# Kernel optimization log

Hardware: AMD Instinct MI355X
Metric: run time of the kernel (lower is better)

The kernel has to match this reference:

```python
import jax, jax.numpy as jnp
import numpy as np

EMBED_DIM = 768
NUM_HEADS = 12
LN_EPS = 1e-5


def _apply_rope3d(p16, e):
    """3-axis RoPE. p16: [B,1,L,3] float16 coords; e: [B,H,L,D] float32.
    Heads split into 3 groups (x/y/z); within each group last dim split in halves
    and rotated by angle coord*freqs (computed in fp16, matching the .half() cast)."""
    B, H, L, D = e.shape
    half = D // 2
    freqs = (10000.0 ** (-jnp.arange(half, dtype=jnp.float32) / half)).astype(jnp.float16)
    ang = p16[..., None] * freqs                     # [B,1,L,3,half] fp16
    ang = jnp.transpose(ang, (0, 3, 1, 2, 4))        # [B,3,1,L,half]
    c, s = jnp.cos(ang), jnp.sin(ang)                # fp16
    eg = e.reshape(B, 3, H // 3, L, D)               # 3 head groups
    e1, e2 = eg[..., :half], eg[..., half:]
    o1 = e1 * c - e2 * s                             # fp16*fp32 -> fp32
    o2 = e2 * c + e1 * s
    return jnp.concatenate([o1, o2], axis=-1).reshape(B, H, L, D)


def setup_inputs() -> dict:
    key = jax.random.key(0)
    ks = jax.random.split(key, 5)
    B, L, C = 4, 2048, EMBED_DIM
    feat = jax.random.normal(ks[0], (B, L, C), dtype=jnp.float32)
    pos = jax.random.normal(ks[1], (B, L, 3), dtype=jnp.float32)
    w_qkv = jax.random.normal(ks[2], (C, 3 * C), dtype=jnp.float32) * (1.0 / np.sqrt(C))
    b_qkv = jnp.zeros((3 * C,), dtype=jnp.float32)
    w_proj = jax.random.normal(ks[3], (C, C), dtype=jnp.float32) * (1.0 / np.sqrt(C))
    b_proj = jnp.zeros((C,), dtype=jnp.float32)
    ln_g = jnp.ones((C,), dtype=jnp.float32)
    ln_b = jnp.zeros((C,), dtype=jnp.float32)
    return {"feat": feat, "pos": pos, "ln_g": ln_g, "ln_b": ln_b,
            "w_qkv": w_qkv, "b_qkv": b_qkv, "w_proj": w_proj, "b_proj": b_proj}


def reference(feat, pos, ln_g, ln_b, w_qkv, b_qkv, w_proj, b_proj):
    B, L, C = feat.shape
    H = NUM_HEADS
    D = C // H
    # LayerNorm
    mu = jnp.mean(feat, axis=-1, keepdims=True)
    var = jnp.mean(jnp.square(feat - mu), axis=-1, keepdims=True)
    x = (feat - mu) * jax.lax.rsqrt(var + LN_EPS) * ln_g + ln_b
    # QKV projection and head split
    qkv = x @ w_qkv + b_qkv
    q, k, v = jnp.split(qkv, 3, axis=-1)
    q = q.reshape(B, L, H, D).transpose(0, 2, 1, 3)  # [B,H,L,D]
    k = k.reshape(B, L, H, D).transpose(0, 2, 1, 3)
    v = v.reshape(B, L, H, D).transpose(0, 2, 1, 3)
    # 3D-coordinate RoPE (angles in fp16 per original .half() cast)
    p16 = pos.astype(jnp.float16)[:, None]           # [B,1,L,3]
    q = _apply_rope3d(p16, q)
    k = _apply_rope3d(p16, k)
    # flex_attention with block_mask=None -> full softmax attention, scale 1/sqrt(D)
    scale = 1.0 / np.sqrt(D)
    att = jax.nn.softmax(jnp.einsum('bhqd,bhkd->bhqk', q, k) * scale, axis=-1)
    out = jnp.einsum('bhqk,bhkd->bhqd', att, v)
    out = out.transpose(0, 2, 1, 3).reshape(B, L, C)
    # output projection (dropout = identity in eval)
    return out @ w_proj + b_proj
```

## Files before the change

kernel.cpp:

```cpp
#include <hip/hip_runtime.h>

typedef unsigned short u16;
typedef unsigned int u32;
typedef __attribute__((ext_vector_type(8))) __bf16 bf16x8;
typedef __attribute__((ext_vector_type(4))) __bf16 bf16x4;
typedef __attribute__((ext_vector_type(8))) u16 ushort8;
typedef __attribute__((ext_vector_type(4))) float f32x4;

#define DEV static __device__ __forceinline__

DEV float bf2f(u16 v) { union { u32 u; float f; } x; x.u = ((u32)v) << 16; return x.f; }
DEV u16 f2bf(float f) {
  u32 u = __builtin_bit_cast(u32, f);
  return (u16)((u + 0x7fffu + ((u >> 16) & 1u)) >> 16);
}
DEV float rnd_bf(float f) { return bf2f(f2bf(f)); }
DEV u32 pack2(float a, float b) { return (u32)f2bf(a) | ((u32)f2bf(b) << 16); }

DEV void gload_lds16(const void* g, void* l) {
  __builtin_amdgcn_global_load_lds((const __attribute__((address_space(1))) u32*)g,
                                   (__attribute__((address_space(3))) u32*)l, 16, 0, 0);
}

DEV f32x4 MFMA16(bf16x8 a, bf16x8 b, f32x4 c) {
  return __builtin_amdgcn_mfma_f32_16x16x32_bf16(a, b, c, 0, 0, 0);
}

#define QSCALE (0.125f * 1.442695040888963f)

__global__ __launch_bounds__(256) void prep_kernel(const float* __restrict__ pos, float2* __restrict__ tab,
                                                   const float* __restrict__ w_qkv, u16* __restrict__ wqkvT,
                                                   const float* __restrict__ w_proj, u16* __restrict__ wprojT,
                                                   const float* __restrict__ feat, const float* __restrict__ gam,
                                                   const float* __restrict__ bet, u16* __restrict__ xo) {
  __shared__ u16 t[64][65];
  const int tid = threadIdx.x;
  const int blk = blockIdx.x;

  if (blk < 3072) {
    int gid = blk * 256 + tid;
    int row = gid & 8191;
    int ad = gid >> 13;
    int axis = ad >> 5, d = ad & 31;
    float p = pos[(size_t)row * 3 + axis];
    float fr = exp2f((float)d * -0.41524101186092029f);
    _Float16 ah = (_Float16)p * (_Float16)fr;
    float sn, cs;
    sincosf((float)ah, &sn, &cs);
    tab[gid] = make_float2((float)(_Float16)cs, (float)(_Float16)sn);
  } else if (blk < 3648) {
    const float* W;
    u16* Wt;
    int rows = 768, cols, bx, by;
    if (blk < 3504) {
      int i2 = blk - 3072;
      W = w_qkv; Wt = wqkvT; cols = 2304; bx = i2 % 36; by = i2 / 36;
    } else {
      int i2 = blk - 3504;
      W = w_proj; Wt = wprojT; cols = 768; bx = i2 % 12; by = i2 / 12;
    }
    const int tr = by << 6, tc = bx << 6;
    {
      int r = tid >> 2, c0 = (tid & 3) << 4;
      const float* src = W + (size_t)(tr + r) * cols + tc + c0;
#pragma unroll
      for (int i = 0; i < 16; i += 4) {
        float4 v = *(const float4*)(src + i);
        t[r][c0 + i]     = f2bf(v.x);
        t[r][c0 + i + 1] = f2bf(v.y);
        t[r][c0 + i + 2] = f2bf(v.z);
        t[r][c0 + i + 3] = f2bf(v.w);
      }
    }
    __syncthreads();
    {
      int dd = tid >> 2, l0 = (tid & 3) << 4;
      ushort8 o0, o1;
#pragma unroll
      for (int i = 0; i < 8; ++i) { o0[i] = t[l0 + i][dd]; o1[i] = t[l0 + 8 + i][dd]; }
      u16* dst = Wt + (size_t)(tc + dd) * rows + tr + l0;
      *(ushort8*)dst = o0;
      *(ushort8*)(dst + 8) = o1;
    }
  } else {
    const int row = (blk - 3648) * 4 + (tid >> 6);
    const int lane = tid & 63;
    const float* f = feat + (size_t)row * 768 + lane * 4;
    float4 v0 = *(const float4*)f;
    float4 v1 = *(const float4*)(f + 256);
    float4 v2 = *(const float4*)(f + 512);
    float s = v0.x + v0.y + v0.z + v0.w + v1.x + v1.y + v1.z + v1.w + v2.x + v2.y + v2.z + v2.w;
    float s2 = v0.x*v0.x + v0.y*v0.y + v0.z*v0.z + v0.w*v0.w
             + v1.x*v1.x + v1.y*v1.y + v1.z*v1.z + v1.w*v1.w
             + v2.x*v2.x + v2.y*v2.y + v2.z*v2.z + v2.w*v2.w;
#pragma unroll
    for (int off = 32; off > 0; off >>= 1) { s += __shfl_xor(s, off); s2 += __shfl_xor(s2, off); }
    const float mu = s * (1.0f / 768.0f);
    const float rstd = rsqrtf(s2 * (1.0f / 768.0f) - mu * mu + 1e-5f);
    u16* o = xo + (size_t)row * 768 + lane * 4;
    const float4* gp = (const float4*)(gam + lane * 4);
    const float4* bp = (const float4*)(bet + lane * 4);
    float4 vv[3] = {v0, v1, v2};
#pragma unroll
    for (int jj = 0; jj < 3; ++jj) {
      float4 gg = gp[jj * 64];
      float4 bb = bp[jj * 64];
      uint2 pk;
      pk.x = pack2((vv[jj].x - mu) * rstd * gg.x + bb.x, (vv[jj].y - mu) * rstd * gg.y + bb.y);
      pk.y = pack2((vv[jj].z - mu) * rstd * gg.z + bb.z, (vv[jj].w - mu) * rstd * gg.w + bb.w);
      *(uint2*)(o + jj * 256) = pk;
    }
  }
}

template<bool ROPE, bool F32OUT, int TM>
__global__ __launch_bounds__(256) void gemm_bt(const u16* __restrict__ A, const u16* __restrict__ Bt,
                                               const float* __restrict__ bias, void* __restrict__ Cout,
                                               u16* __restrict__ Qb, u16* __restrict__ Kb,
                                               const float2* __restrict__ tab, int M, int N, int K) {
  __shared__ u16 lds[TM * 64 + 8192];
  constexpr int MF = TM / 32;
  const int tid = threadIdx.x;
  const int lane = tid & 63, wv = tid >> 6;
  const int l16 = lane & 15, g = lane >> 4;
  const int nt = N >> 7;
  int bid = (int)blockIdx.x;
  { const int cpx = (int)gridDim.x >> 3; bid = (bid & 7) * cpx + (bid >> 3); }
  const int bm = bid / nt, bn = bid % nt;
  const int m0 = bm * TM, n0 = bn << 7;
  const int wr = (wv >> 1) * (TM / 2), wc = (wv & 1) << 6;
  const int rl = wv * 8 + (lane >> 3);
  const int slot = lane & 7;

  f32x4 acc[MF][4] = {};

  for (int k0 = 0; k0 < K; k0 += 64) {
    __syncthreads();
#pragma unroll
    for (int it = 0; it < TM / 32; ++it) {
      int r = it * 32 + rl;
      gload_lds16(A + (size_t)(m0 + r) * K + k0 + 8 * (slot ^ (r & 7)),
                  (char*)lds + it * 4096 + wv * 1024);
    }
#pragma unroll
    for (int it = 0; it < 4; ++it) {
      int r = it * 32 + rl;
      gload_lds16(Bt + (size_t)(n0 + r) * K + k0 + 8 * (slot ^ (r & 7)),
                  (char*)lds + TM * 128 + it * 4096 + wv * 1024);
    }
    __syncthreads();
#pragma unroll
    for (int ks = 0; ks < 2; ++ks) {
      bf16x8 af[MF], bfr[4];
#pragma unroll
      for (int mf = 0; mf < MF; ++mf) {
        int r = wr + mf * 16 + l16;
        af[mf] = *(const bf16x8*)((const char*)lds + r * 128 + ((ks * 64 + g * 16) ^ ((r & 7) << 4)));
      }
#pragma unroll
      for (int nf = 0; nf < 4; ++nf) {
        int r = wc + nf * 16 + l16;
        bfr[nf] = *(const bf16x8*)((const char*)lds + TM * 128 + r * 128 + ((ks * 64 + g * 16) ^ ((r & 7) << 4)));
      }
#pragma unroll
      for (int mf = 0; mf < MF; ++mf)
#pragma unroll
        for (int nf = 0; nf < 4; ++nf)
          acc[mf][nf] = MFMA16(af[mf], bfr[nf], acc[mf][nf]);
    }
  }

  bool ropePath = false;
  if constexpr (ROPE) ropePath = (n0 < 1536);
  if (ropePath) {
    if constexpr (ROPE) {
      const int colbase = n0 + wc;
      const bool isQ = colbase < 768;
      const int h = (isQ ? colbase : colbase - 768) >> 6;
      const int axis = h >> 2;
      u16* P = isQ ? Qb : Kb;
#pragma unroll
      for (int nf = 0; nf < 2; ++nf) {
        const int col = n0 + wc + nf * 16 + l16;
        const int d = nf * 16 + l16;
        const float2* trow = tab + (size_t)(axis * 32 + d) * 8192;
        const float b1 = bias[col], b2 = bias[col + 32];
#pragma unroll
        for (int mf = 0; mf < MF; ++mf) {
          int row0 = m0 + wr + mf * 16 + g * 4;
#pragma unroll
          for (int j = 0; j < 4; ++j) {
            int row = row0 + j;
            float2 cs2 = trow[row];
            float c = cs2.x, s = cs2.y;
            float a = acc[mf][nf][j] + b1;
            float bb = acc[mf][nf + 2][j] + b2;
            float o1 = a * c - bb * s;
            float o2 = bb * c + a * s;
            if (isQ) { o1 *= QSCALE; o2 *= QSCALE; }
            size_t obase = ((size_t)((row >> 11) * 12 + h) * 2048 + (row & 2047)) * 64;
            P[obase + d]      = f2bf(o1);
            P[obase + d + 32] = f2bf(o2);
          }
        }
      }
    }
  } else {
    const int colsub = (ROPE ? 1536 : 0);
    const int Nout = (ROPE ? 768 : N);
#pragma unroll
    for (int nf = 0; nf < 4; ++nf) {
      int col = n0 + wc + nf * 16 + l16;
      float bb = bias[col];
#pragma unroll
      for (int mf = 0; mf < MF; ++mf) {
        int row = m0 + wr + mf * 16 + g * 4;
#pragma unroll
        for (int j = 0; j < 4; ++j) {
          float v = acc[mf][nf][j] + bb;
          if (F32OUT) ((float*)Cout)[(size_t)(row + j) * Nout + col - colsub] = rnd_bf(v);
          else        ((u16*)Cout)[(size_t)(row + j) * Nout + col - colsub] = f2bf(v);
        }
      }
    }
  }
}

__global__ __launch_bounds__(256) void v_transpose(const u16* __restrict__ Vp, u16* __restrict__ Vt) {
  __shared__ u16 t[64][65];
  const int tid = threadIdx.x;
  const int lt = blockIdx.x, bh = blockIdx.y;
  const int b = bh / 12, h = bh - b * 12;
  {
    int r = tid >> 2, c0 = (tid & 3) << 4;
    const u16* src = Vp + (size_t)(b * 2048 + lt * 64 + r) * 768 + h * 64 + c0;
    ushort8 a0 = *(const ushort8*)src;
    ushort8 a1 = *(const ushort8*)(src + 8);
#pragma unroll
    for (int i = 0; i < 8; ++i) { t[r][c0 + i] = a0[i]; t[r][c0 + 8 + i] = a1[i]; }
  }
  __syncthreads();
  {
    int dd = tid >> 2, l0 = (tid & 3) << 4;
    ushort8 o0, o1;
#pragma unroll
    for (int i = 0; i < 8; ++i) { o0[i] = t[l0 + i][dd]; o1[i] = t[l0 + 8 + i][dd]; }
    u16* dst = Vt + (size_t)(bh * 64 + dd) * 2048 + lt * 64 + l0;
    *(ushort8*)dst = o0;
    *(ushort8*)(dst + 8) = o1;
  }
}

__global__ __launch_bounds__(256) void attn_kernel(const u16* __restrict__ Q, const u16* __restrict__ K,
                                                   const u16* __restrict__ Vt, u16* __restrict__ O) {
  __shared__ u16 kv_lds[3][8192];
  const int tid = threadIdx.x;
  const int lane = tid & 63, wv = tid >> 6;
  const int l16 = lane & 15, g = lane >> 4;
  int bid = (int)blockIdx.x;
  bid = (bid & 7) * 96 + (bid >> 3);
  const int bh = bid >> 4;
  const int q0 = (bid & 15) * 128 + wv * 32;
  const size_t base = (size_t)bh * (2048 * 64);
  const size_t vbase = (size_t)bh * (64 * 2048);
  const int rl = wv * 8 + (lane >> 3);
  const int slot = lane & 7;

  bf16x8 qf[2][2];
#pragma unroll
  for (int qm = 0; qm < 2; ++qm)
#pragma unroll
    for (int ks = 0; ks < 2; ++ks)
      qf[qm][ks] = *(const bf16x8*)(Q + base + (size_t)(q0 + qm * 16 + l16) * 64 + ks * 32 + g * 8);

  float lsum[2] = {0.f, 0.f};
  f32x4 oacc[2][4] = {};

  auto STAGE = [&](int tile, int buf) {
#pragma unroll
    for (int it = 0; it < 2; ++it) {
      int r = it * 32 + rl;
      gload_lds16(K + base + (size_t)(tile * 64 + r) * 64 + 8 * (slot ^ (r & 7)),
                  (char*)kv_lds + buf * 16384 + it * 4096 + wv * 1024);
      gload_lds16(Vt + vbase + (size_t)r * 2048 + tile * 64 + 8 * (slot ^ (r & 7)),
                  (char*)kv_lds + buf * 16384 + 8192 + it * 4096 + wv * 1024);
    }
  };

  STAGE(0, 0);
  STAGE(1, 1);
  asm volatile("s_waitcnt vmcnt(4)" ::: "memory");
  __builtin_amdgcn_s_barrier();

  for (int t = 0; t < 32; ++t) {
    if (t < 30) STAGE(t + 2, (t + 2) % 3);

    const char* kb = (const char*)kv_lds + (t % 3) * 16384;
    const char* vbuf = kb + 8192;

    f32x4 st[2][4] = {};
#pragma unroll
    for (int ks = 0; ks < 2; ++ks) {
      bf16x8 kf[4];
#pragma unroll
      for (int n = 0; n < 4; ++n) {
        int r = n * 16 + l16;
        kf[n] = *(const bf16x8*)(kb + r * 128 + ((ks * 64 + g * 16) ^ ((r & 7) << 4)));
      }
      __builtin_amdgcn_s_setprio(1);
#pragma unroll
      for (int qm = 0; qm < 2; ++qm)
#pragma unroll
        for (int n = 0; n < 4; ++n)
          st[qm][n] = MFMA16(kf[n], qf[qm][ks], st[qm][n]);
      __builtin_amdgcn_s_setprio(0);
    }

#pragma unroll
    for (int ks2 = 0; ks2 < 2; ++ks2) {
      bf16x8 vf[4];
#pragma unroll
      for (int db = 0; db < 4; ++db) {
        int r = db * 16 + l16;
        int swz = (r & 7) << 4;
        const char* rowb = vbuf + r * 128;
        bf16x4 lo = *(const bf16x4*)(rowb + ((ks2 * 64 + g * 8) ^ swz));
        bf16x4 hi = *(const bf16x4*)(rowb + ((ks2 * 64 + g * 8 + 32) ^ swz));
        vf[db] = __builtin_shufflevector(lo, hi, 0, 1, 2, 3, 4, 5, 6, 7);
      }
      bf16x8 pf[2];
#pragma unroll
      for (int qm = 0; qm < 2; ++qm) {
        float e[8];
#pragma unroll
        for (int j = 0; j < 4; ++j) {
          e[j]     = __builtin_amdgcn_exp2f(st[qm][2 * ks2][j]);
          e[4 + j] = __builtin_amdgcn_exp2f(st[qm][2 * ks2 + 1][j]);
        }
        lsum[qm] += ((e[0] + e[1]) + (e[2] + e[3])) + ((e[4] + e[5]) + (e[6] + e[7]));
        bf16x8 pv;
#pragma unroll
        for (int j = 0; j < 8; ++j) pv[j] = (__bf16)e[j];
        pf[qm] = pv;
      }
      __builtin_amdgcn_s_setprio(1);
#pragma unroll
      for (int qm = 0; qm < 2; ++qm)
#pragma unroll
        for (int db = 0; db < 4; ++db)
          oacc[qm][db] = MFMA16(vf[db], pf[qm], oacc[qm][db]);
      __builtin_amdgcn_s_setprio(0);
    }

    if (t < 31) {
      if (t < 30) asm volatile("s_waitcnt vmcnt(4)" ::: "memory");
      else        asm volatile("s_waitcnt vmcnt(0)" ::: "memory");
      __builtin_amdgcn_s_barrier();
    }
  }

  const int b = bh / 12, h = bh - b * 12;
#pragma unroll
  for (int qm = 0; qm < 2; ++qm) {
    float tot = lsum[qm];
    tot += __shfl_xor(tot, 16);
    tot += __shfl_xor(tot, 32);
    float inv = 1.0f / tot;
    size_t row = (size_t)b * 2048 + q0 + qm * 16 + l16;
#pragma unroll
    for (int db = 0; db < 4; ++db) {
      uint2 pk;
      pk.x = pack2(oacc[qm][db][0] * inv, oacc[qm][db][1] * inv);
      pk.y = pack2(oacc[qm][db][2] * inv, oacc[qm][db][3] * inv);
      *(uint2*)(O + row * 768 + h * 64 + db * 16 + g * 4) = pk;
    }
  }
}

extern "C" void kernel_launch(void* const* d_in, const int* in_sizes, int n_in,
                              void* d_out, int out_size, void* d_ws, size_t ws_size,
                              hipStream_t stream) {
  (void)in_sizes; (void)n_in; (void)out_size; (void)ws_size;
  const float* feat   = (const float*)d_in[0];
  const float* pos    = (const float*)d_in[1];
  const float* ln_g   = (const float*)d_in[2];
  const float* ln_b   = (const float*)d_in[3];
  const float* w_qkv  = (const float*)d_in[4];
  const float* b_qkv  = (const float*)d_in[5];
  const float* w_proj = (const float*)d_in[6];
  const float* b_proj = (const float*)d_in[7];
  float* out = (float*)d_out;
  char* ws = (char*)d_ws;
  u16* xln    = (u16*)(ws);
  u16* wqkvT  = (u16*)(ws + 12582912);
  u16* wprojT = (u16*)(ws + 16121856);
  u16* Qb     = (u16*)(ws + 17301504);
  u16* Kb     = (u16*)(ws + 29884416);
  u16* Vp     = (u16*)(ws + 42467328);
  u16* Vtb    = (u16*)(ws + 55050240);
  u16* attnout= (u16*)(ws + 67633152);
  float2* tab = (float2*)(ws + 80216064);

  prep_kernel<<<5696, 256, 0, stream>>>(pos, tab, w_qkv, wqkvT, w_proj, wprojT, feat, ln_g, ln_b, xln);
  gemm_bt<true, false, 128><<<1152, 256, 0, stream>>>(xln, wqkvT, b_qkv, Vp, Qb, Kb, tab, 8192, 2304, 768);
  v_transpose<<<dim3(32, 48), 256, 0, stream>>>(Vp, Vtb);
  attn_kernel<<<768, 256, 0, stream>>>(Qb, Kb, Vtb, attnout);
  gemm_bt<false, true, 64><<<768, 256, 0, stream>>>(attnout, wprojT, b_proj, out, nullptr, nullptr, nullptr, 8192, 768, 768);
}
```

Measured before the change: 163.4 us.

## Compute softmax row sums with MFMA and switch attention to double buffering

The softmax denominator is now accumulated by an extra MFMA against a vector of ones, using the bf16-rounded probabilities, instead of per-lane float adds plus a final cross-lane shuffle reduction. The K/V staging changes from a three-buffer ring with explicit vmcnt waits to a two-buffer ping-pong with a full __syncthreads per tile. This cuts LDS use and VALU work but adds matrix-core work and leaves less prefetch depth to hide global-load latency behind compute. The denominator now sums rounded bf16 values, which changes numerics slightly.

```diff
diff --git a/kernel.cpp b/kernel.cpp
--- a/kernel.cpp
+++ b/kernel.cpp
@@ -253,7 +253,7 @@
 
 __global__ __launch_bounds__(256) void attn_kernel(const u16* __restrict__ Q, const u16* __restrict__ K,
                                                    const u16* __restrict__ Vt, u16* __restrict__ O) {
-  __shared__ u16 kv_lds[3][8192];
+  __shared__ u16 kv_lds[2][8192];
   const int tid = threadIdx.x;
   const int lane = tid & 63, wv = tid >> 6;
   const int l16 = lane & 15, g = lane >> 4;
@@ -266,6 +266,10 @@
   const int rl = wv * 8 + (lane >> 3);
   const int slot = lane & 7;
 
+  bf16x8 ones;
+#pragma unroll
+  for (int j = 0; j < 8; ++j) ones[j] = (__bf16)1.0f;
+
   bf16x8 qf[2][2];
 #pragma unroll
   for (int qm = 0; qm < 2; ++qm)
@@ -273,29 +277,33 @@
     for (int ks = 0; ks < 2; ++ks)
       qf[qm][ks] = *(const bf16x8*)(Q + base + (size_t)(q0 + qm * 16 + l16) * 64 + ks * 32 + g * 8);
 
-  float lsum[2] = {0.f, 0.f};
+  f32x4 sacc[2] = {};
   f32x4 oacc[2][4] = {};
 
-  auto STAGE = [&](int tile, int buf) {
-#pragma unroll
-    for (int it = 0; it < 2; ++it) {
-      int r = it * 32 + rl;
-      gload_lds16(K + base + (size_t)(tile * 64 + r) * 64 + 8 * (slot ^ (r & 7)),
-                  (char*)kv_lds + buf * 16384 + it * 4096 + wv * 1024);
-      gload_lds16(Vt + vbase + (size_t)r * 2048 + tile * 64 + 8 * (slot ^ (r & 7)),
-                  (char*)kv_lds + buf * 16384 + 8192 + it * 4096 + wv * 1024);
-    }
-  };
-
-  STAGE(0, 0);
-  STAGE(1, 1);
-  asm volatile("s_waitcnt vmcnt(4)" ::: "memory");
-  __builtin_amdgcn_s_barrier();
-
-  for (int t = 0; t < 32; ++t) {
-    if (t < 30) STAGE(t + 2, (t + 2) % 3);
-
-    const char* kb = (const char*)kv_lds + (t % 3) * 16384;
+#pragma unroll
+  for (int it = 0; it < 2; ++it) {
+    int r = it * 32 + rl;
+    gload_lds16(K + base + (size_t)r * 64 + 8 * (slot ^ (r & 7)),
+                (char*)kv_lds + it * 4096 + wv * 1024);
+    gload_lds16(Vt + vbase + (size_t)r * 2048 + 8 * (slot ^ (r & 7)),
+                (char*)kv_lds + 8192 + it * 4096 + wv * 1024);
+  }
+  __syncthreads();
+
+  int cur = 0;
+  for (int kv0 = 0; kv0 < 2048; kv0 += 64) {
+    if (kv0 + 64 < 2048) {
+#pragma unroll
+      for (int it = 0; it < 2; ++it) {
+        int r = it * 32 + rl;
+        gload_lds16(K + base + (size_t)(kv0 + 64 + r) * 64 + 8 * (slot ^ (r & 7)),
+                    (char*)kv_lds + (cur ^ 1) * 16384 + it * 4096 + wv * 1024);
+        gload_lds16(Vt + vbase + (size_t)r * 2048 + kv0 + 64 + 8 * (slot ^ (r & 7)),
+                    (char*)kv_lds + (cur ^ 1) * 16384 + 8192 + it * 4096 + wv * 1024);
+      }
+    }
+
+    const char* kb = (const char*)kv_lds + cur * 16384;
     const char* vbuf = kb + 8192;
 
     f32x4 st[2][4] = {};
@@ -331,41 +339,33 @@
       bf16x8 pf[2];
 #pragma unroll
       for (int qm = 0; qm < 2; ++qm) {
-        float e[8];
+        bf16x8 pv;
 #pragma unroll
         for (int j = 0; j < 4; ++j) {
-          e[j]     = __builtin_amdgcn_exp2f(st[qm][2 * ks2][j]);
-          e[4 + j] = __builtin_amdgcn_exp2f(st[qm][2 * ks2 + 1][j]);
+          pv[j]     = (__bf16)__builtin_amdgcn_exp2f(st[qm][2 * ks2][j]);
+          pv[4 + j] = (__bf16)__builtin_amdgcn_exp2f(st[qm][2 * ks2 + 1][j]);
         }
-        lsum[qm] += ((e[0] + e[1]) + (e[2] + e[3])) + ((e[4] + e[5]) + (e[6] + e[7]));
-        bf16x8 pv;
-#pragma unroll
-        for (int j = 0; j < 8; ++j) pv[j] = (__bf16)e[j];
         pf[qm] = pv;
       }
       __builtin_amdgcn_s_setprio(1);
 #pragma unroll
-      for (int qm = 0; qm < 2; ++qm)
+      for (int qm = 0; qm < 2; ++qm) {
+        sacc[qm] = MFMA16(ones, pf[qm], sacc[qm]);
 #pragma unroll
         for (int db = 0; db < 4; ++db)
           oacc[qm][db] = MFMA16(vf[db], pf[qm], oacc[qm][db]);
+      }
       __builtin_amdgcn_s_setprio(0);
     }
 
-    if (t < 31) {
-      if (t < 30) asm volatile("s_waitcnt vmcnt(4)" ::: "memory");
-      else        asm volatile("s_waitcnt vmcnt(0)" ::: "memory");
-      __builtin_amdgcn_s_barrier();
-    }
+    __syncthreads();
+    cur ^= 1;
   }
 
   const int b = bh / 12, h = bh - b * 12;
 #pragma unroll
   for (int qm = 0; qm < 2; ++qm) {
-    float tot = lsum[qm];
-    tot += __shfl_xor(tot, 16);
-    tot += __shfl_xor(tot, 32);
-    float inv = 1.0f / tot;
+    float inv = 1.0f / sacc[qm][0];
     size_t row = (size_t)b * 2048 + q0 + qm * 16 + l16;
 #pragma unroll
     for (int db = 0; db < 4; ++db) {
```

Result: faster. 148.5 us (-9.1%).
